# Performance work log

Measured on AMD Instinct MI355X. Metric: run time of the kernel, lower is better.

Reference implementation:

```python
import jax, jax.numpy as jnp
import numpy as np

N, K = 10000, 16
EDGE_DIM, HID = 32, 64
MULT = 8            # rep1.mult == rep2.mult (out_mult)
NL = 2              # lvals [0,1] -> 2 irreps per rep
DIM = 4             # (2*0+1) + (2*1+1)
NHEADS = 4
OUT3 = 3 * MULT     # qkv multiplicity
RW_FLAT = NL * NL * MULT * OUT3   # 768 radial-weight outputs per edge
HEAD_DIM = (MULT * DIM) // NHEADS # 8
INDICES = jnp.array([0, 1, 1, 1]) # irrep index for each of the DIM slots (l=0 then l=1 x3)


def setup_inputs() -> dict:
    key = jax.random.key(0)
    ks = jax.random.split(key, 10)
    rn = lambda i, shape, sc=1.0: (jax.random.normal(ks[i], shape, jnp.float32) * sc)
    return {
        "b1": rn(0, (N, K, DIM, NL)),
        "b2": rn(1, (N, K, NL, DIM)),
        "edge_feats": rn(2, (N, K, EDGE_DIM)),
        "f": rn(3, (N, MULT, DIM)),
        "neighbor_idx": jax.random.randint(ks[4], (N, K), 0, N),
        # RadialWeight MLP params (xavier-ish scales, zero biases as in _init_weights)
        "W1": rn(5, (HID, EDGE_DIM), (2.0 / (HID + EDGE_DIM)) ** 0.5),
        "b1_lin": jnp.zeros((HID,), jnp.float32),
        "W2": rn(6, (RW_FLAT, HID), (2.0 / (RW_FLAT + HID)) ** 0.5),
        "b2_lin": jnp.zeros((RW_FLAT,), jnp.float32),
        # EquivariantLinear out_proj params
        "W_out": rn(7, (NL * MULT, MULT), (2.0 / (NL * MULT + MULT)) ** 0.5),
        "bias_out": jnp.zeros((MULT, 1), jnp.float32),
    }


def reference(b1, b2, edge_feats, f, neighbor_idx, W1, b1_lin, W2, b2_lin, W_out, bias_out):
    E = N * K
    b1f = b1.reshape(E, DIM, NL)
    b2f = b2.reshape(E, NL, DIM)
    ef = edge_feats.reshape(E, EDGE_DIM)

    # RadialWeight: 2-layer MLP with exact GELU -> per-edge tensor-product weights
    h = jax.nn.gelu(ef @ W1.T + b1_lin, approximate=False)          # (E, HID)
    rw = (h @ W2.T + b2_lin).reshape(E, NL * OUT3, NL * MULT)        # (E, 48, 16)

    # EquivariantConvolution: gather src node features, chained small matmuls
    f_src = f[neighbor_idx.reshape(-1)]                              # (E, MULT, DIM)
    tmp = jnp.einsum('emd,edl->eml', f_src, b1f)                     # (E, MULT, NL)
    tmp = jnp.matmul(rw, tmp.reshape(E, NL * MULT, 1))               # (E, NL*OUT3, 1)
    qkv = jnp.matmul(tmp.reshape(E, OUT3, NL), b2f)                  # (E, OUT3, DIM)

    # split into q,k,v heads
    qkv = qkv.reshape(N, K, 3 * MULT, DIM)
    q, k_, v = jnp.split(qkv, 3, axis=2)                             # each (N, K, MULT, DIM)
    qh = q.reshape(N, K, NHEADS, HEAD_DIM)
    kh = k_.reshape(N, K, NHEADS, HEAD_DIM)
    vh = v.reshape(N, K, NHEADS, HEAD_DIM)

    # per-edge attention, softmax over the k neighbors
    scale = HEAD_DIM ** -0.5
    scores = jnp.einsum('nkhd,nkhd->nkh', qh, kh) * scale            # (N, K, NHEADS)
    attn = jax.nn.softmax(scores, axis=1)
    out = jnp.einsum('nkh,nkhd->nhd', attn, vh).reshape(N, MULT, DIM)

    # EquivariantLinear out_proj: per-irrep mixing over multiplicity channels
    o = jnp.einsum('om,nmd->nod', W_out, out).reshape(N, NL, MULT, DIM)
    idx = jnp.broadcast_to(INDICES[None, None, None, :], (N, 1, MULT, DIM))
    o = jnp.take_along_axis(o, idx, axis=1)[:, 0]                    # (N, MULT, DIM)
    # bias only on the scalar (l=0) slot; activation is Identity in out_proj
    o = o.at[:, :, 0].add(bias_out[:, 0])
    return o
```

## Files before the change

### kernel.cpp

```cpp
#include <hip/hip_runtime.h>
#include <math.h>

#define E_TOT   160000
#define BE      64
#define TPB     256
#define NBLK    (E_TOT / BE)
#define TV_OFF  16384
#define T2S     52
#define SMEM_SZ 20480

typedef __attribute__((ext_vector_type(8))) __bf16 bf16x8;
typedef __attribute__((ext_vector_type(4))) float f32x4;

static __device__ __forceinline__ unsigned short f2bf(float v) {
    unsigned int u = __float_as_uint(v);
    u += 0x7FFFu + ((u >> 16) & 1u);
    return (unsigned short)(u >> 16);
}
static __device__ __forceinline__ float bf2f(unsigned int s) {
    return __uint_as_float(s << 16);
}

static __device__ __forceinline__ float gelu_exact(float a) {
    float x = a * 0.70710678118654752f;
    float s = fabsf(x);
    float t = __builtin_amdgcn_rcpf(fmaf(0.3275911f, s, 1.0f));
    float p = fmaf(1.061405429f, t, -1.453152027f);
    p = fmaf(p, t, 1.421413741f);
    p = fmaf(p, t, -0.284496736f);
    p = fmaf(p, t, 0.254829592f);
    p = p * t;
    float er = fmaf(-p, __expf(-s * s), 1.0f);
    er = copysignf(er, x);
    return 0.5f * a * (1.0f + er);
}

__global__ __launch_bounds__(256) void w_split(
    const float* __restrict__ W2, const float* __restrict__ b2l,
    uint4* __restrict__ hi4, uint4* __restrict__ lo4, uint4* __restrict__ bb4)
{
    const int c = blockIdx.x * 256 + threadIdx.x;
    if (c < 6144) {
        const int lane = c & 63, rest = c >> 6;
        const int kk   = rest & 1, tj = rest >> 1;
        const int j    = tj & 15,  t  = tj >> 4;
        const int grp  = lane >> 4, r16 = lane & 15;
        const float* src = W2 + (size_t)((t * 16 + r16) * 16 + j) * 64 + kk * 32 + grp * 8;
        union { uint4 u; unsigned short s[8]; } H, L;
        #pragma unroll
        for (int i = 0; i < 8; ++i) {
            float w = src[i];
            unsigned short h = f2bf(w);
            H.s[i] = h;
            L.s[i] = f2bf(w - bf2f(h));
        }
        hi4[c] = H.u;
        lo4[c] = L.u;
    } else if (c < 6144 + 192) {
        const int cc   = c - 6144;
        const int lane = cc & 63, t = cc >> 6;
        const int grp  = lane >> 4, r16 = lane & 15;
        union { uint4 u; unsigned short s[8]; } B;
        #pragma unroll
        for (int i = 0; i < 8; ++i)
            B.s[i] = (grp < 2) ? f2bf(b2l[(t * 16 + r16) * 16 + grp * 8 + i])
                               : (unsigned short)0;
        bb4[cc] = B.u;
    }
}

__global__ __launch_bounds__(TPB, 2) void eq_attn_kernel(
    const float* __restrict__ b1,
    const float* __restrict__ b2,
    const float* __restrict__ ef,
    const float* __restrict__ f,
    const int*   __restrict__ nidx,
    const float* __restrict__ W1,
    const float* __restrict__ b1l,
    const float* __restrict__ Wout,
    const float* __restrict__ bias,
    const uint4* __restrict__ wsh,
    const uint4* __restrict__ wsl,
    const uint4* __restrict__ bb,
    float* __restrict__ out)
{
    __shared__ unsigned char smem[SMEM_SZ];
    const int tid = threadIdx.x;
    const int p   = tid >> 6;
    const int el  = tid & 63;
    const int r16 = el & 15;
    const int grp = el >> 4;
    const int e0  = blockIdx.x * BE;
    const int e   = e0 + el;

    {
        float efr[32];
        const float4* ef4 = reinterpret_cast<const float4*>(ef + (size_t)e * 32);
        #pragma unroll
        for (int i = 0; i < 8; ++i) {
            float4 v = ef4[i];
            efr[i*4+0] = v.x; efr[i*4+1] = v.y; efr[i*4+2] = v.z; efr[i*4+3] = v.w;
        }
        #pragma unroll
        for (int cc = 0; cc < 2; ++cc) {
            const int c8 = 2 * p + cc;
            union { uint4 u; unsigned short s[8]; } H, L;
            #pragma unroll
            for (int i = 0; i < 8; ++i) {
                const int hid = c8 * 8 + i;
                float acc1 = b1l[hid];
                #pragma unroll
                for (int c = 0; c < 32; ++c)
                    acc1 = fmaf(efr[c], W1[hid * 32 + c], acc1);
                float v = gelu_exact(acc1);
                unsigned short hs = f2bf(v);
                H.s[i] = hs;
                L.s[i] = f2bf(v - bf2f(hs));
            }
            const int ch = c8 ^ (el & 7);
            *(uint4*)(smem +        el * 128 + ch * 16) = H.u;
            *(uint4*)(smem + 8192 + el * 128 + ch * 16) = L.u;
        }
    }
    {
        const int src = nidx[e];
        float b1r[8];
        const float4* b14 = reinterpret_cast<const float4*>(b1 + (size_t)e * 8);
        float4 u0 = b14[0], u1 = b14[1];
        b1r[0]=u0.x; b1r[1]=u0.y; b1r[2]=u0.z; b1r[3]=u0.w;
        b1r[4]=u1.x; b1r[5]=u1.y; b1r[6]=u1.z; b1r[7]=u1.w;
        float* tvp = (float*)(smem + TV_OFF);
        const float4* f4 = reinterpret_cast<const float4*>(f + (size_t)src * 32);
        #pragma unroll
        for (int mm = 0; mm < 2; ++mm) {
            const int m = 2 * p + mm;
            float4 v = f4[m];
            float a0 = v.x * b1r[0] + v.y * b1r[2] + v.z * b1r[4] + v.w * b1r[6];
            float a1 = v.x * b1r[1] + v.y * b1r[3] + v.z * b1r[5] + v.w * b1r[7];
            tvp[(m*2+0) * 64 + el] = a0;
            tvp[(m*2+1) * 64 + el] = a1;
        }
    }

    __syncthreads();

    bf16x8 Ah0, Ah1, Al0, Al1;
    {
        const int row = p * 16 + r16;
        const int ch0 = grp ^ (r16 & 7);
        const int ch1 = (4 + grp) ^ (r16 & 7);
        Ah0 = *(const bf16x8*)(smem +        row * 128 + ch0 * 16);
        Ah1 = *(const bf16x8*)(smem +        row * 128 + ch1 * 16);
        Al0 = *(const bf16x8*)(smem + 8192 + row * 128 + ch0 * 16);
        Al1 = *(const bf16x8*)(smem + 8192 + row * 128 + ch1 * 16);
    }

    f32x4 acc[3];
    {
        const float* tvp = (const float*)(smem + TV_OFF);
        union { uint4 u; unsigned short s[8]; } P;
        #pragma unroll
        for (int i = 0; i < 8; ++i) {
            float v = (grp < 2) ? tvp[(grp * 8 + i) * 64 + p * 16 + r16] : 0.0f;
            P.s[i] = f2bf(v);
        }
        bf16x8 tvb = *(bf16x8*)&P.u;
        #pragma unroll
        for (int t = 0; t < 3; ++t) {
            uint4 u = bb[t * 64 + el];
            bf16x8 blb = *(bf16x8*)&u;
            acc[t] = __builtin_amdgcn_mfma_f32_16x16x32_bf16(
                tvb, blb, (f32x4){0.f, 0.f, 0.f, 0.f}, 0, 0, 0);
        }
    }

    const float4* tv4 = (const float4*)(smem + TV_OFF);
    #pragma unroll 2
    for (int j = 0; j < 16; ++j) {
        bf16x8 Bhi[3][2], Blo[3][2];
        #pragma unroll
        for (int t = 0; t < 3; ++t)
            #pragma unroll
            for (int kk = 0; kk < 2; ++kk) {
                const int chunk = ((t * 16 + j) * 2 + kk) * 64 + el;
                Bhi[t][kk] = ((const bf16x8*)wsh)[chunk];
                Blo[t][kk] = ((const bf16x8*)wsl)[chunk];
            }
        float4 tv = tv4[j * 16 + p * 4 + grp];
        #pragma unroll
        for (int t = 0; t < 3; ++t) {
            f32x4 rw = (f32x4){0.f, 0.f, 0.f, 0.f};
            rw = __builtin_amdgcn_mfma_f32_16x16x32_bf16(Ah0, Bhi[t][0], rw, 0, 0, 0);
            rw = __builtin_amdgcn_mfma_f32_16x16x32_bf16(Ah1, Bhi[t][1], rw, 0, 0, 0);
            rw = __builtin_amdgcn_mfma_f32_16x16x32_bf16(Al0, Bhi[t][0], rw, 0, 0, 0);
            rw = __builtin_amdgcn_mfma_f32_16x16x32_bf16(Al1, Bhi[t][1], rw, 0, 0, 0);
            rw = __builtin_amdgcn_mfma_f32_16x16x32_bf16(Ah0, Blo[t][0], rw, 0, 0, 0);
            rw = __builtin_amdgcn_mfma_f32_16x16x32_bf16(Ah1, Blo[t][1], rw, 0, 0, 0);
            acc[t].x = fmaf(tv.x, rw.x, acc[t].x);
            acc[t].y = fmaf(tv.y, rw.y, acc[t].y);
            acc[t].z = fmaf(tv.z, rw.z, acc[t].z);
            acc[t].w = fmaf(tv.w, rw.w, acc[t].w);
        }
    }

    __syncthreads();

    {
        float* t2p = (float*)smem;
        const int eb = p * 16 + grp * 4;
        #pragma unroll
        for (int t = 0; t < 3; ++t) {
            t2p[(eb + 0) * T2S + t * 16 + r16] = acc[t].x;
            t2p[(eb + 1) * T2S + t * 16 + r16] = acc[t].y;
            t2p[(eb + 2) * T2S + t * 16 + r16] = acc[t].z;
            t2p[(eb + 3) * T2S + t * 16 + r16] = acc[t].w;
        }
    }
    __syncthreads();

    if (el < 16) {
        const int erow = p * 16 + el;
        const int ec   = e0 + erow;
        float t2[48];
        {
            const float* t2r = (const float*)smem + (size_t)erow * T2S;
            #pragma unroll
            for (int o2 = 0; o2 < 48; ++o2) t2[o2] = t2r[o2];
        }
        float b2r[8];
        {
            const float4* b24 = reinterpret_cast<const float4*>(b2 + (size_t)ec * 8);
            float4 u0 = b24[0], u1 = b24[1];
            b2r[0]=u0.x; b2r[1]=u0.y; b2r[2]=u0.z; b2r[3]=u0.w;
            b2r[4]=u1.x; b2r[5]=u1.y; b2r[6]=u1.z; b2r[7]=u1.w;
        }
        float q[8][4];
        #pragma unroll
        for (int o = 0; o < 8; ++o) {
            float t0 = t2[2*o+0], t1 = t2[2*o+1];
            #pragma unroll
            for (int d = 0; d < 4; ++d)
                q[o][d] = fmaf(t0, b2r[d], t1 * b2r[4+d]);
        }
        float scores[4] = {0.f, 0.f, 0.f, 0.f};
        #pragma unroll
        for (int o = 0; o < 8; ++o) {
            float t0 = t2[16+2*o+0], t1 = t2[16+2*o+1];
            float sacc = 0.f;
            #pragma unroll
            for (int d = 0; d < 4; ++d) {
                float kr = fmaf(t0, b2r[d], t1 * b2r[4+d]);
                sacc = fmaf(q[o][d], kr, sacc);
            }
            scores[o >> 1] += sacc;
        }
        float vv[8][4];
        #pragma unroll
        for (int o = 0; o < 8; ++o) {
            float t0 = t2[32+2*o+0], t1 = t2[32+2*o+1];
            #pragma unroll
            for (int d = 0; d < 4; ++d)
                vv[o][d] = fmaf(t0, b2r[d], t1 * b2r[4+d]);
        }
        float attn[4];
        #pragma unroll
        for (int hh = 0; hh < 4; ++hh) {
            float s = scores[hh] * 0.35355339059327373f;
            float mx = s;
            #pragma unroll
            for (int msk = 8; msk; msk >>= 1)
                mx = fmaxf(mx, __shfl_xor(mx, msk, 16));
            float pr = __expf(s - mx);
            float ps = pr;
            #pragma unroll
            for (int msk = 8; msk; msk >>= 1)
                ps += __shfl_xor(ps, msk, 16);
            attn[hh] = pr / ps;
        }
        float osum[8][4];
        #pragma unroll
        for (int m = 0; m < 8; ++m) {
            float w = attn[m >> 1];
            #pragma unroll
            for (int d = 0; d < 4; ++d) {
                float val = w * vv[m][d];
                #pragma unroll
                for (int msk = 8; msk; msk >>= 1)
                    val += __shfl_xor(val, msk, 16);
                osum[m][d] = val;
            }
        }
        if (el == 0) {
            const int n = ec >> 4;
            #pragma unroll
            for (int od = 0; od < 8; ++od) {
                #pragma unroll
                for (int d = 0; d < 4; ++d) {
                    const int row = (d == 0) ? od : (8 + od);
                    float a = (d == 0) ? bias[od] : 0.f;
                    #pragma unroll
                    for (int m = 0; m < 8; ++m)
                        a = fmaf(Wout[row * 8 + m], osum[m][d], a);
                    out[(size_t)n * 32 + od * 4 + d] = a;
                }
            }
        }
    }
}

extern "C" void kernel_launch(void* const* d_in, const int* in_sizes, int n_in,
                              void* d_out, int out_size, void* d_ws, size_t ws_size,
                              hipStream_t stream) {
    const float* b1   = (const float*)d_in[0];
    const float* b2   = (const float*)d_in[1];
    const float* ef   = (const float*)d_in[2];
    const float* f    = (const float*)d_in[3];
    const int*   nidx = (const int*)d_in[4];
    const float* W1   = (const float*)d_in[5];
    const float* b1l  = (const float*)d_in[6];
    const float* W2   = (const float*)d_in[7];
    const float* b2l  = (const float*)d_in[8];
    const float* Wout = (const float*)d_in[9];
    const float* bias = (const float*)d_in[10];
    float* out = (float*)d_out;

    uint4* wsh = (uint4*)d_ws;
    uint4* wsl = wsh + 6144;
    uint4* bb  = wsh + 12288;

    hipLaunchKernelGGL(w_split, dim3(25), dim3(256), 0, stream, W2, b2l, wsh, wsl, bb);
    hipLaunchKernelGGL(eq_attn_kernel, dim3(NBLK), dim3(TPB), 0, stream,
                       b1, b2, ef, f, nidx, W1, b1l, Wout, bias,
                       (const uint4*)wsh, (const uint4*)wsl, (const uint4*)bb, out);
}
```

Before: 201.2 us.

## Split radial-weight reduction over j across waves and reduce partials in LDS

Each wave now handles 4 of the 16 hidden-chunk indices j for all four 16-edge tiles, instead of all 16 j for one tile. Each wave therefore loads only its own quarter of the W2 hi/lo fragments, which cuts per-wave global/L2 weight traffic by four. The four partial accumulators are combined through a rotating store-then-add sequence in shared memory with extra barriers. Launch bounds are raised to 4 blocks per CU, which constrains registers even though acc now holds 12 vectors and A fragments are reloaded from LDS per tile.

```diff
diff --git a/kernel.cpp b/kernel.cpp
--- a/kernel.cpp
+++ b/kernel.cpp
@@ -69,7 +69,28 @@
     }
 }
 
-__global__ __launch_bounds__(TPB, 2) void eq_attn_kernel(
+#define RED_STORE(S)                                                \
+    {                                                               \
+        _Pragma("unroll")                                           \
+        for (int t = 0; t < 3; ++t) {                               \
+            t2p[(eb + 0) * T2S + t * 16 + r16] = acc[S][t].x;       \
+            t2p[(eb + 1) * T2S + t * 16 + r16] = acc[S][t].y;       \
+            t2p[(eb + 2) * T2S + t * 16 + r16] = acc[S][t].z;       \
+            t2p[(eb + 3) * T2S + t * 16 + r16] = acc[S][t].w;       \
+        }                                                           \
+    }
+#define RED_ADD(S)                                                  \
+    {                                                               \
+        _Pragma("unroll")                                           \
+        for (int t = 0; t < 3; ++t) {                               \
+            t2p[(eb + 0) * T2S + t * 16 + r16] += acc[S][t].x;      \
+            t2p[(eb + 1) * T2S + t * 16 + r16] += acc[S][t].y;      \
+            t2p[(eb + 2) * T2S + t * 16 + r16] += acc[S][t].z;      \
+            t2p[(eb + 3) * T2S + t * 16 + r16] += acc[S][t].w;      \
+        }                                                           \
+    }
+
+__global__ __launch_bounds__(TPB, 4) void eq_attn_kernel(
     const float* __restrict__ b1,
     const float* __restrict__ b2,
     const float* __restrict__ ef,
@@ -144,39 +165,41 @@
 
     __syncthreads();
 
-    bf16x8 Ah0, Ah1, Al0, Al1;
-    {
-        const int row = p * 16 + r16;
-        const int ch0 = grp ^ (r16 & 7);
-        const int ch1 = (4 + grp) ^ (r16 & 7);
-        Ah0 = *(const bf16x8*)(smem +        row * 128 + ch0 * 16);
-        Ah1 = *(const bf16x8*)(smem +        row * 128 + ch1 * 16);
-        Al0 = *(const bf16x8*)(smem + 8192 + row * 128 + ch0 * 16);
-        Al1 = *(const bf16x8*)(smem + 8192 + row * 128 + ch1 * 16);
-    }
-
-    f32x4 acc[3];
-    {
+    f32x4 acc[4][3];
+    if (p == 0) {
         const float* tvp = (const float*)(smem + TV_OFF);
-        union { uint4 u; unsigned short s[8]; } P;
-        #pragma unroll
-        for (int i = 0; i < 8; ++i) {
-            float v = (grp < 2) ? tvp[(grp * 8 + i) * 64 + p * 16 + r16] : 0.0f;
-            P.s[i] = f2bf(v);
-        }
-        bf16x8 tvb = *(bf16x8*)&P.u;
+        bf16x8 blb[3];
         #pragma unroll
         for (int t = 0; t < 3; ++t) {
             uint4 u = bb[t * 64 + el];
-            bf16x8 blb = *(bf16x8*)&u;
-            acc[t] = __builtin_amdgcn_mfma_f32_16x16x32_bf16(
-                tvb, blb, (f32x4){0.f, 0.f, 0.f, 0.f}, 0, 0, 0);
-        }
+            blb[t] = *(bf16x8*)&u;
+        }
+        #pragma unroll
+        for (int s = 0; s < 4; ++s) {
+            union { uint4 u; unsigned short sh[8]; } P;
+            #pragma unroll
+            for (int i = 0; i < 8; ++i) {
+                float v = (grp < 2) ? tvp[(grp * 8 + i) * 64 + s * 16 + r16] : 0.0f;
+                P.sh[i] = f2bf(v);
+            }
+            bf16x8 tvb = *(bf16x8*)&P.u;
+            #pragma unroll
+            for (int t = 0; t < 3; ++t)
+                acc[s][t] = __builtin_amdgcn_mfma_f32_16x16x32_bf16(
+                    tvb, blb[t], (f32x4){0.f, 0.f, 0.f, 0.f}, 0, 0, 0);
+        }
+    } else {
+        #pragma unroll
+        for (int s = 0; s < 4; ++s)
+            #pragma unroll
+            for (int t = 0; t < 3; ++t)
+                acc[s][t] = (f32x4){0.f, 0.f, 0.f, 0.f};
     }
 
     const float4* tv4 = (const float4*)(smem + TV_OFF);
-    #pragma unroll 2
-    for (int j = 0; j < 16; ++j) {
+    #pragma unroll
+    for (int jj = 0; jj < 4; ++jj) {
+        const int j = p * 4 + jj;
         bf16x8 Bhi[3][2], Blo[3][2];
         #pragma unroll
         for (int t = 0; t < 3; ++t)
@@ -186,20 +209,31 @@
                 Bhi[t][kk] = ((const bf16x8*)wsh)[chunk];
                 Blo[t][kk] = ((const bf16x8*)wsl)[chunk];
             }
-        float4 tv = tv4[j * 16 + p * 4 + grp];
-        #pragma unroll
-        for (int t = 0; t < 3; ++t) {
-            f32x4 rw = (f32x4){0.f, 0.f, 0.f, 0.f};
-            rw = __builtin_amdgcn_mfma_f32_16x16x32_bf16(Ah0, Bhi[t][0], rw, 0, 0, 0);
-            rw = __builtin_amdgcn_mfma_f32_16x16x32_bf16(Ah1, Bhi[t][1], rw, 0, 0, 0);
-            rw = __builtin_amdgcn_mfma_f32_16x16x32_bf16(Al0, Bhi[t][0], rw, 0, 0, 0);
-            rw = __builtin_amdgcn_mfma_f32_16x16x32_bf16(Al1, Bhi[t][1], rw, 0, 0, 0);
-            rw = __builtin_amdgcn_mfma_f32_16x16x32_bf16(Ah0, Blo[t][0], rw, 0, 0, 0);
-            rw = __builtin_amdgcn_mfma_f32_16x16x32_bf16(Ah1, Blo[t][1], rw, 0, 0, 0);
-            acc[t].x = fmaf(tv.x, rw.x, acc[t].x);
-            acc[t].y = fmaf(tv.y, rw.y, acc[t].y);
-            acc[t].z = fmaf(tv.z, rw.z, acc[t].z);
-            acc[t].w = fmaf(tv.w, rw.w, acc[t].w);
+        #pragma unroll
+        for (int s = 0; s < 4; ++s) {
+            const int mt  = (p + s) & 3;
+            const int row = mt * 16 + r16;
+            const int ch0 = grp ^ (r16 & 7);
+            const int ch1 = (4 + grp) ^ (r16 & 7);
+            bf16x8 Ah0 = *(const bf16x8*)(smem +        row * 128 + ch0 * 16);
+            bf16x8 Ah1 = *(const bf16x8*)(smem +        row * 128 + ch1 * 16);
+            bf16x8 Al0 = *(const bf16x8*)(smem + 8192 + row * 128 + ch0 * 16);
+            bf16x8 Al1 = *(const bf16x8*)(smem + 8192 + row * 128 + ch1 * 16);
+            float4 tv = tv4[j * 16 + mt * 4 + grp];
+            #pragma unroll
+            for (int t = 0; t < 3; ++t) {
+                f32x4 rw = (f32x4){0.f, 0.f, 0.f, 0.f};
+                rw = __builtin_amdgcn_mfma_f32_16x16x32_bf16(Ah0, Bhi[t][0], rw, 0, 0, 0);
+                rw = __builtin_amdgcn_mfma_f32_16x16x32_bf16(Ah1, Bhi[t][1], rw, 0, 0, 0);
+                rw = __builtin_amdgcn_mfma_f32_16x16x32_bf16(Al0, Bhi[t][0], rw, 0, 0, 0);
+                rw = __builtin_amdgcn_mfma_f32_16x16x32_bf16(Al1, Bhi[t][1], rw, 0, 0, 0);
+                rw = __builtin_amdgcn_mfma_f32_16x16x32_bf16(Ah0, Blo[t][0], rw, 0, 0, 0);
+                rw = __builtin_amdgcn_mfma_f32_16x16x32_bf16(Ah1, Blo[t][1], rw, 0, 0, 0);
+                acc[s][t].x = fmaf(tv.x, rw.x, acc[s][t].x);
+                acc[s][t].y = fmaf(tv.y, rw.y, acc[s][t].y);
+                acc[s][t].z = fmaf(tv.z, rw.z, acc[s][t].z);
+                acc[s][t].w = fmaf(tv.w, rw.w, acc[s][t].w);
+            }
         }
     }
 
@@ -207,16 +241,27 @@
 
     {
         float* t2p = (float*)smem;
-        const int eb = p * 16 + grp * 4;
-        #pragma unroll
-        for (int t = 0; t < 3; ++t) {
-            t2p[(eb + 0) * T2S + t * 16 + r16] = acc[t].x;
-            t2p[(eb + 1) * T2S + t * 16 + r16] = acc[t].y;
-            t2p[(eb + 2) * T2S + t * 16 + r16] = acc[t].z;
-            t2p[(eb + 3) * T2S + t * 16 + r16] = acc[t].w;
-        }
-    }
-    __syncthreads();
+        {
+            const int eb = p * 16 + grp * 4;
+            RED_STORE(0);
+        }
+        __syncthreads();
+        {
+            const int eb = (((p + 1) & 3) * 16) + grp * 4;
+            RED_ADD(1);
+        }
+        __syncthreads();
+        {
+            const int eb = (((p + 2) & 3) * 16) + grp * 4;
+            RED_ADD(2);
+        }
+        __syncthreads();
+        {
+            const int eb = (((p + 3) & 3) * 16) + grp * 4;
+            RED_ADD(3);
+        }
+        __syncthreads();
+    }
 
     if (el < 16) {
         const int erow = p * 16 + el;
```

New measurement: 306.0 us. 52.1% more time.

## Stage radial-weight B fragments through double-buffered LDS with async global-to-LDS loads

Applied to the files above, without the earlier changes.

Each of the four waves previously loaded all twelve hi/lo weight fragments per iteration straight from global memory, so every wave re-read the same data. Now each wave issues global_load_lds for a quarter of the fragments into a double-buffered LDS region, prefetching the next j step while the MFMAs for the current step run, with a block barrier each iteration. Shared memory per block grows to about 44 KB and launch bounds rise to 3 blocks per CU. The trade is 16 extra barriers per block and a dependence on async LDS writes landing before the barrier, which requires the right waitcnt handling.

```diff
diff --git a/kernel.cpp b/kernel.cpp
--- a/kernel.cpp
+++ b/kernel.cpp
@@ -6,8 +6,9 @@
 #define TPB     256
 #define NBLK    (E_TOT / BE)
 #define TV_OFF  16384
+#define BS_OFF  20480
 #define T2S     52
-#define SMEM_SZ 20480
+#define SMEM_SZ 45056
 
 typedef __attribute__((ext_vector_type(8))) __bf16 bf16x8;
 typedef __attribute__((ext_vector_type(4))) float f32x4;
@@ -69,7 +70,19 @@
     }
 }
 
-__global__ __launch_bounds__(TPB, 2) void eq_attn_kernel(
+#define STAGE(BUF, J)                                                               \
+    {                                                                               \
+        _Pragma("unroll")                                                           \
+        for (int tt = 0; tt < 3; ++tt) {                                            \
+            const uint4* gsrc = wsx + ((size_t)(((tt * 16 + (J)) * 2 + kks) * 64) + el); \
+            __builtin_amdgcn_global_load_lds(                                       \
+                (const __attribute__((address_space(1))) unsigned int*)(const void*)gsrc, \
+                (__attribute__((address_space(3))) unsigned int*)(void*)(smem + BS_OFF + (BUF) * 12288 + (tt * 4 + kks * 2 + hls) * 1024), \
+                16, 0, 0);                                                          \
+        }                                                                           \
+    }
+
+__global__ __launch_bounds__(TPB, 3) void eq_attn_kernel(
     const float* __restrict__ b1,
     const float* __restrict__ b2,
     const float* __restrict__ ef,
@@ -93,6 +106,11 @@
     const int e0  = blockIdx.x * BE;
     const int e   = e0 + el;
 
+    const int kks = p >> 1, hls = p & 1;
+    const uint4* wsx = hls ? wsl : wsh;
+
+    STAGE(0, 0);
+
     {
         float efr[32];
         const float4* ef4 = reinterpret_cast<const float4*>(ef + (size_t)e * 32);
@@ -158,11 +176,11 @@
     f32x4 acc[3];
     {
         const float* tvp = (const float*)(smem + TV_OFF);
-        union { uint4 u; unsigned short s[8]; } P;
+        union { uint4 u; unsigned short sh[8]; } P;
         #pragma unroll
         for (int i = 0; i < 8; ++i) {
             float v = (grp < 2) ? tvp[(grp * 8 + i) * 64 + p * 16 + r16] : 0.0f;
-            P.s[i] = f2bf(v);
+            P.sh[i] = f2bf(v);
         }
         bf16x8 tvb = *(bf16x8*)&P.u;
         #pragma unroll
@@ -175,35 +193,34 @@
     }
 
     const float4* tv4 = (const float4*)(smem + TV_OFF);
-    #pragma unroll 2
+    int cur = 0;
     for (int j = 0; j < 16; ++j) {
-        bf16x8 Bhi[3][2], Blo[3][2];
-        #pragma unroll
-        for (int t = 0; t < 3; ++t)
-            #pragma unroll
-            for (int kk = 0; kk < 2; ++kk) {
-                const int chunk = ((t * 16 + j) * 2 + kk) * 64 + el;
-                Bhi[t][kk] = ((const bf16x8*)wsh)[chunk];
-                Blo[t][kk] = ((const bf16x8*)wsl)[chunk];
-            }
+        if (j < 15) STAGE(cur ^ 1, j + 1);
+
+        const unsigned char* bcur = smem + BS_OFF + cur * 12288 + el * 16;
         float4 tv = tv4[j * 16 + p * 4 + grp];
         #pragma unroll
         for (int t = 0; t < 3; ++t) {
+            bf16x8 Bh0 = *(const bf16x8*)(bcur + (t * 4 + 0) * 1024);
+            bf16x8 Bl0 = *(const bf16x8*)(bcur + (t * 4 + 1) * 1024);
+            bf16x8 Bh1 = *(const bf16x8*)(bcur + (t * 4 + 2) * 1024);
+            bf16x8 Bl1 = *(const bf16x8*)(bcur + (t * 4 + 3) * 1024);
             f32x4 rw = (f32x4){0.f, 0.f, 0.f, 0.f};
-            rw = __builtin_amdgcn_mfma_f32_16x16x32_bf16(Ah0, Bhi[t][0], rw, 0, 0, 0);
-            rw = __builtin_amdgcn_mfma_f32_16x16x32_bf16(Ah1, Bhi[t][1], rw, 0, 0, 0);
-            rw = __builtin_amdgcn_mfma_f32_16x16x32_bf16(Al0, Bhi[t][0], rw, 0, 0, 0);
-            rw = __builtin_amdgcn_mfma_f32_16x16x32_bf16(Al1, Bhi[t][1], rw, 0, 0, 0);
-            rw = __builtin_amdgcn_mfma_f32_16x16x32_bf16(Ah0, Blo[t][0], rw, 0, 0, 0);
-            rw = __builtin_amdgcn_mfma_f32_16x16x32_bf16(Ah1, Blo[t][1], rw, 0, 0, 0);
+            rw = __builtin_amdgcn_mfma_f32_16x16x32_bf16(Ah0, Bh0, rw, 0, 0, 0);
+            rw = __builtin_amdgcn_mfma_f32_16x16x32_bf16(Ah1, Bh1, rw, 0, 0, 0);
+            rw = __builtin_amdgcn_mfma_f32_16x16x32_bf16(Al0, Bh0, rw, 0, 0, 0);
+            rw = __builtin_amdgcn_mfma_f32_16x16x32_bf16(Al1, Bh1, rw, 0, 0, 0);
+            rw = __builtin_amdgcn_mfma_f32_16x16x32_bf16(Ah0, Bl0, rw, 0, 0, 0);
+            rw = __builtin_amdgcn_mfma_f32_16x16x32_bf16(Ah1, Bl1, rw, 0, 0, 0);
             acc[t].x = fmaf(tv.x, rw.x, acc[t].x);
             acc[t].y = fmaf(tv.y, rw.y, acc[t].y);
             acc[t].z = fmaf(tv.z, rw.z, acc[t].z);
             acc[t].w = fmaf(tv.w, rw.w, acc[t].w);
         }
-    }
-
-    __syncthreads();
+
+        __syncthreads();
+        cur ^= 1;
+    }
 
     {
         float* t2p = (float*)smem;
@@ -326,10 +343,10 @@
 
     uint4* wsh = (uint4*)d_ws;
     uint4* wsl = wsh + 6144;
-    uint4* bb  = wsh + 12288;
-
-    hipLaunchKernelGGL(w_split, dim3(25), dim3(256), 0, stream, W2, b2l, wsh, wsl, bb);
+    uint4* bbp = wsh + 12288;
+
+    hipLaunchKernelGGL(w_split, dim3(25), dim3(256), 0, stream, W2, b2l, wsh, wsl, bbp);
     hipLaunchKernelGGL(eq_attn_kernel, dim3(NBLK), dim3(TPB), 0, stream,
                        b1, b2, ef, f, nidx, W1, b1l, Wout, bias,
-                       (const uint4*)wsh, (const uint4*)wsl, (const uint4*)bb, out);
-}
+                       (const uint4*)wsh, (const uint4*)wsl, (const uint4*)bbp, out);
+}
```

New measurement: 217.8 us. 1.08x slower.
